# Kernel optimization log

Measured on AMD Instinct MI355X. Metric: run time of the kernel, lower is better.

Reference implementation:

```python
import jax, jax.numpy as jnp
import numpy as np

N = 50000      # nodes
E = 1600000    # edges
F = 128        # num_feature
H = 256        # num_hidden
L = 3          # num_message_passing_steps
EPS = 1e-5     # LayerNorm eps (torch default)


def setup_inputs() -> dict:
    key = jax.random.key(0)
    ks = jax.random.split(key, 8)
    node = jax.random.normal(ks[0], (N, F), dtype=jnp.float32)
    edges = jax.random.randint(ks[1], (2, E), 0, N, dtype=jnp.int64)
    edges_attr = jax.random.uniform(ks[2], (E,), dtype=jnp.float32)
    sF = np.float32(1.0 / np.sqrt(F))
    sH = np.float32(1.0 / np.sqrt(H))
    W1 = jax.random.normal(ks[3], (F, H), dtype=jnp.float32) * sF
    b1 = jnp.zeros((H,), jnp.float32)
    W_convs = jax.random.normal(ks[4], (L, H, H), dtype=jnp.float32) * sH
    b_convs = jnp.zeros((L, H), jnp.float32)
    ln_g = jnp.ones((L, H), jnp.float32)
    ln_b = jnp.zeros((L, H), jnp.float32)
    fc_W = jax.random.normal(ks[5], (H, 2), dtype=jnp.float32) * sH
    fc_b = jnp.zeros((2,), jnp.float32)
    return dict(node=node, edges=edges, edges_attr=edges_attr, W1=W1, b1=b1,
                W_convs=W_convs, b_convs=b_convs, ln_g=ln_g, ln_b=ln_b,
                fc_W=fc_W, fc_b=fc_b)


def gcn_conv(x, src_a, dst_a, w_a, W, b):
    # PyG GCNConv: x' = D^-1/2 (A + I) D^-1/2 (x W) + b, edge weights w.
    # src_a/dst_a/w_a already include self-loops (weight 1).
    n = x.shape[0]
    xw = x @ W                                      # [N, H]
    deg = jax.ops.segment_sum(w_a, dst_a, num_segments=n)
    deg_safe = jnp.where(deg > 0, deg, 1.0)
    dinv = jnp.where(deg > 0, jax.lax.rsqrt(deg_safe), 0.0)
    norm = dinv[src_a] * w_a * dinv[dst_a]          # [E+N]
    msg = xw[src_a] * norm[:, None]                 # gather + scale
    out = jax.ops.segment_sum(msg, dst_a, num_segments=n)  # scatter-add
    return out + b


def layer_norm(x, g, b):
    mu = jnp.mean(x, axis=-1, keepdims=True)
    var = jnp.mean((x - mu) ** 2, axis=-1, keepdims=True)
    return (x - mu) * jax.lax.rsqrt(var + EPS) * g + b


def reference(node, edges, edges_attr, W1, b1, W_convs, b_convs, ln_g, ln_b, fc_W, fc_b):
    n = node.shape[0]
    loop = jnp.arange(n, dtype=edges.dtype)
    src_a = jnp.concatenate([edges[0], loop])
    dst_a = jnp.concatenate([edges[1], loop])
    w_a = jnp.concatenate([edges_attr, jnp.ones((n,), edges_attr.dtype)])

    x = gcn_conv(node, src_a, dst_a, w_a, W1, b1)
    for i in range(L):
        x_res = x
        x = gcn_conv(x, src_a, dst_a, w_a, W_convs[i], b_convs[i])
        x = layer_norm(x, ln_g[i], ln_b[i])
        x = jax.nn.relu(x + x_res)
    x = x @ fc_W + fc_b                              # [N, 2]
    return jnp.mean(x, axis=0, keepdims=True)        # global_mean_pool, batch=None -> [1, 2]
```

## Files before the change

kernel.cpp:

```cpp
#include <hip/hip_runtime.h>

#define EPS 1e-5f
#define FIXSCALE 8388608.0f
#define NBK 64

typedef __attribute__((ext_vector_type(8))) short short8;
typedef __attribute__((ext_vector_type(4))) short short4v;
typedef __attribute__((ext_vector_type(4))) float float4v;
typedef __attribute__((ext_vector_type(2))) float float2v;
typedef __attribute__((ext_vector_type(8))) unsigned short ushort8;
typedef __attribute__((ext_vector_type(4))) unsigned int uint4v;

#if __has_builtin(__builtin_nontemporal_load)
#define NT_LOAD(p) __builtin_nontemporal_load(p)
#else
#define NT_LOAD(p) (*(p))
#endif

__device__ __forceinline__ unsigned short f2b(float f) {
    union { float f; unsigned u; } v; v.f = f;
    unsigned r = v.u + 0x7FFF + ((v.u >> 16) & 1);
    return (unsigned short)(r >> 16);
}
__device__ __forceinline__ float b2f(unsigned short u) {
    union { unsigned u; float f; } v; v.u = ((unsigned)u) << 16;
    return v.f;
}

__device__ __forceinline__ int qbucket(int cnt) {
    int qc = ((cnt + 4) & ~3) >> 2;
    return qc < NBK - 1 ? qc : NBK - 1;
}


__global__ __launch_bounds__(256) void rank_kernel(const int* __restrict__ dst,
                                                   const float* __restrict__ w,
                                                   unsigned long long* __restrict__ combo,
                                                   int* __restrict__ rank, int E) {
    int e = blockIdx.x * 256 + threadIdx.x;
    if (e < E) {
        int d = dst[e];
        unsigned long long pack = (1ULL << 32) | (unsigned long long)(unsigned)(w[e] * FIXSCALE);
        unsigned long long old = atomicAdd(&combo[(size_t)d * 8], pack);
        rank[e] = (int)(old >> 32);
    }
}

__global__ __launch_bounds__(256) void dinv_kernel(const unsigned long long* __restrict__ combo,
                                                   float* __restrict__ dinv, int n) {
    int d = blockIdx.x * 256 + threadIdx.x;
    if (d < n) {
        float degv = (float)(unsigned)(combo[(size_t)d * 8] & 0xffffffffULL) * (1.0f / FIXSCALE);
        dinv[d] = rsqrtf(degv + 1.0f);
    }
}


__global__ __launch_bounds__(256) void bin_hist_kernel(const unsigned long long* __restrict__ combo,
                                                       int* __restrict__ blockhist, int n) {
    __shared__ int lh[NBK];
    int t = threadIdx.x;
    if (t < NBK) lh[t] = 0;
    __syncthreads();
    int d = blockIdx.x * 256 + t;
    if (d < n) {
        int cnt = (int)(combo[(size_t)d * 8] >> 32);
        atomicAdd(&lh[qbucket(cnt)], 1);
    }
    __syncthreads();
    if (t < NBK) blockhist[blockIdx.x * NBK + t] = lh[t];
}

__global__ __launch_bounds__(256) void bin_prescan_kernel(const int* __restrict__ blockhist,
                                                          int* __restrict__ blockpre,
                                                          int* __restrict__ tot, int nblk) {
    int bkt = blockIdx.x;
    int t = threadIdx.x, lane = t & 63, w = t >> 6;
    __shared__ int wsum[4];
    __shared__ int s_carry;
    if (t == 0) s_carry = 0;
    __syncthreads();
    for (int base = 0; base < nblk; base += 256) {
        int i = base + t;
        int v = (i < nblk) ? blockhist[i * NBK + bkt] : 0;
        int x = v;
        for (int off = 1; off < 64; off <<= 1) {
            int u = __shfl_up(x, off);
            if (lane >= off) x += u;
        }
        if (lane == 63) wsum[w] = x;
        __syncthreads();
        if (t == 0) {
            int a = wsum[0];
            wsum[0] = 0;
            for (int k = 1; k < 4; ++k) { int b = wsum[k]; wsum[k] = a; a += b; }
            wsum[0] = 0;
        }
        __syncthreads();
        int carry = s_carry;
        int woff = wsum[w];
        if (i < nblk) blockpre[i * NBK + bkt] = carry + woff + x - v;
        __syncthreads();
        if (t == 255) s_carry = carry + woff + x;
        __syncthreads();
    }
    if (t == 0) tot[bkt] = s_carry;
}

__global__ __launch_bounds__(64) void bin_suffix_kernel(const int* __restrict__ tot,
                                                        int* __restrict__ base) {
    int t = threadIdx.x;
    int v = tot[t];
    int s = v;
    for (int off = 1; off < 64; off <<= 1) {
        int u = __shfl_down(s, off);
        if (t + off < 64) s += u;
    }
    base[t] = s - v;
}

__global__ __launch_bounds__(256) void bin_scatter_kernel(const unsigned long long* __restrict__ combo,
                                                          const int* __restrict__ base,
                                                          const int* __restrict__ blockpre,
                                                          int* __restrict__ perm,
                                                          int* __restrict__ posod,
                                                          int* __restrict__ qlen, int n) {
    __shared__ int lcur[NBK];
    int t = threadIdx.x;
    if (t < NBK) lcur[t] = base[t] + blockpre[blockIdx.x * NBK + t];
    __syncthreads();
    int d = blockIdx.x * 256 + t;
    if (d < n) {
        int cnt = (int)(combo[(size_t)d * 8] >> 32);
        int pos = atomicAdd(&lcur[qbucket(cnt)], 1);
        perm[pos] = d;
        posod[d] = pos;
        qlen[pos] = (cnt + 4) & ~3;
    }
}

__global__ __launch_bounds__(1024) void scan_kernel(const int* __restrict__ qlen,
                                                    int* __restrict__ row_ptr, int n) {
    int tid = threadIdx.x, lane = tid & 63, w = tid >> 6;
    __shared__ int wsum[16];
    __shared__ int s_carry;
    if (tid == 0) s_carry = 0;
    __syncthreads();
    for (int base = 0; base < n; base += 1024) {
        int i = base + tid;
        int v = (i < n) ? qlen[i] : 0;
        int x = v;
        for (int off = 1; off < 64; off <<= 1) {
            int t = __shfl_up(x, off);
            if (lane >= off) x += t;
        }
        if (lane == 63) wsum[w] = x;
        __syncthreads();
        if (w == 0 && lane < 16) {
            int s = wsum[lane];
            for (int off = 1; off < 16; off <<= 1) {
                int t = __shfl_up(s, off, 16);
                if (lane >= off) s += t;
            }
            wsum[lane] = s;
        }
        __syncthreads();
        int carry = s_carry;
        int woff = (w > 0) ? wsum[w - 1] : 0;
        if (i < n) row_ptr[i + 1] = carry + woff + x;
        __syncthreads();
        if (tid == 0) s_carry = carry + wsum[15];
        __syncthreads();
    }
    if (tid == 0) row_ptr[0] = 0;
}

__global__ __launch_bounds__(256) void selfpad_kernel(const unsigned long long* __restrict__ combo,
                                                      const int* __restrict__ row_ptr,
                                                      const int* __restrict__ posod,
                                                      const float* __restrict__ dinv,
                                                      unsigned int* __restrict__ edge, int n) {
    int d = blockIdx.x * 256 + threadIdx.x;
    if (d < n) {
        int cnt = (int)(combo[(size_t)d * 8] >> 32);
        int slot = posod[d];
        int j0 = row_ptr[slot], j1 = row_ptr[slot + 1];
        float di = dinv[d];
        edge[j0] = ((unsigned)f2b(di * di) << 16) | (unsigned)slot;
        for (int j = j0 + 1 + cnt; j < j1; ++j) edge[j] = (unsigned)slot;
    }
}

__global__ __launch_bounds__(256) void scatter2_kernel(
    const int* __restrict__ src, const int* __restrict__ dst,
    const float* __restrict__ w, const int* __restrict__ rank,
    const int* __restrict__ row_ptr, const int* __restrict__ posod,
    const float* __restrict__ dinv, unsigned int* __restrict__ edge, int E) {
    int e = blockIdx.x * 256 + threadIdx.x;
    if (e < E) {
        int d = dst[e], s = src[e];
        float wn = dinv[s] * w[e] * dinv[d];
        edge[row_ptr[posod[d]] + 1 + rank[e]] = ((unsigned)f2b(wn) << 16) | (unsigned)posod[s];
    }
}

__global__ __launch_bounds__(256) void cast_sliced_kernel(const float* __restrict__ in,
                                                          const int* __restrict__ perm,
                                                          unsigned short* __restrict__ out,
                                                          int n, int F) {
    int idx = blockIdx.x * 256 + threadIdx.x;
    if (idx < n * (F / 4)) {
        int f4 = idx * 4;
        int slot = f4 / F, f = f4 - slot * F;
        float4 v = *(const float4*)&in[(size_t)perm[slot] * F + f];
        short4v s = (short4v){(short)f2b(v.x), (short)f2b(v.y), (short)f2b(v.z), (short)f2b(v.w)};
        *(short4v*)&out[((size_t)(f >> 5) * n + slot) * 32 + (f & 31)] = s;
    }
}

__global__ __launch_bounds__(256) void wtrans_kernel(const float* __restrict__ W,
                                                     unsigned short* __restrict__ Wt,
                                                     int K, int Nc) {
    int o = blockIdx.x * 256 + threadIdx.x;
    if (o < K * Nc) {
        int n = o / K, k = o - n * K;
        Wt[o] = f2b(W[(size_t)k * Nc + n]);
    }
}


#define GST 88

template <bool SLICEOUT>
__global__ __launch_bounds__(256) void gemm_n256(const unsigned short* __restrict__ A,
                                                 const unsigned short* __restrict__ Bt,
                                                 unsigned short* __restrict__ Cout,
                                                 const float* __restrict__ bias,
                                                 int M, int K) {
    __shared__ __align__(16) short As[64 * GST];
    __shared__ __align__(16) short Bs[256 * GST];
    int t = threadIdx.x;
    int lane = t & 63, w = t >> 6;
    int quad = lane >> 4, l16 = lane & 15;
    int row0 = blockIdx.x * 64;

    float4v acc[16];
#pragma unroll
    for (int c = 0; c < 16; ++c) acc[c] = (float4v){0.f, 0.f, 0.f, 0.f};

    int arow = t >> 2, ak16 = (t & 3) * 16;
    int bcol0 = t >> 2, bko = (t & 3) * 16;

    for (int k_outer = 0; k_outer < K; k_outer += 64) {
        bool rowok = (row0 + arow) < M;
        const unsigned short* ap = &A[(size_t)(row0 + arow) * K + k_outer + ak16];
        uint4 z = make_uint4(0, 0, 0, 0);
        uint4 u0 = rowok ? *(const uint4*)ap : z;
        uint4 u1 = rowok ? *(const uint4*)(ap + 8) : z;
        *(uint4*)&As[arow * GST + ak16] = u0;
        *(uint4*)&As[arow * GST + ak16 + 8] = u1;
#pragma unroll
        for (int cb = 0; cb < 4; ++cb) {
            int col = bcol0 + 64 * cb;
            const unsigned short* bp = &Bt[(size_t)col * K + k_outer + bko];
#pragma unroll
            for (int u = 0; u < 2; ++u)
                *(uint4*)&Bs[col * GST + bko + u * 8] = *(const uint4*)&bp[u * 8];
        }
        __syncthreads();
#pragma unroll
        for (int k0 = 0; k0 < 64; k0 += 32) {
            short8 a = *(const short8*)&As[(w * 16 + l16) * GST + k0 + quad * 8];
#pragma unroll
            for (int c = 0; c < 16; ++c) {
                short8 b = *(const short8*)&Bs[(c * 16 + l16) * GST + k0 + quad * 8];
                acc[c] = __builtin_amdgcn_mfma_f32_16x16x32_bf16(a, b, acc[c], 0, 0, 0);
            }
        }
        __syncthreads();
    }
#pragma unroll
    for (int c = 0; c < 16; ++c) {
        int col = c * 16 + l16;
        float bcol = (!SLICEOUT) ? bias[col] : 0.0f;
#pragma unroll
        for (int r = 0; r < 4; ++r) {
            int row = row0 + w * 16 + quad * 4 + r;
            if (row < M) {
                if (SLICEOUT)
                    Cout[((size_t)(c >> 1) * M + row) * 32 + ((c & 1) << 4) + l16] = f2b(acc[c][r]);
                else
                    Cout[(size_t)row * 256 + col] = f2b(acc[c][r] + bcol);
            }
        }
    }
}


#define CAPQ 2048

template <int CSH>
__global__ __launch_bounds__(256) void agg_grp(
    const unsigned short* __restrict__ tab0, const int* __restrict__ row_ptr,
    const unsigned int* __restrict__ edge, unsigned short* __restrict__ outb, int n) {
    __shared__ uint4v eq[CAPQ];
    int b = blockIdx.x;
    int s = b & ((1 << CSH) - 1);
    int grp = b >> CSH;
    int t = threadIdx.x;
    int d0 = grp * 64;
    int d = d0 + (t >> 2);

    const uint4v* e4p = (const uint4v*)edge;
    int qbase = row_ptr[d0] >> 2;
    int dmax = d0 + 64 < n ? d0 + 64 : n;
    int qcnt = (row_ptr[dmax] >> 2) - qbase;
    int qstage = qcnt < CAPQ ? qcnt : CAPQ;
    for (int i = t; i < qstage; i += 256) eq[i] = NT_LOAD(&e4p[qbase + i]);
    __syncthreads();

    if (d >= n) return;
    int fo = (t & 3) << 3;
    const unsigned short* tab = tab0 + (size_t)s * n * 32;

    int j = row_ptr[d] >> 2, j1 = row_ptr[d + 1] >> 2;
    int jmid = j1 < qbase + CAPQ ? j1 : qbase + CAPQ;

    float2v a2[4];
#pragma unroll
    for (int k = 0; k < 4; ++k) a2[k] = (float2v){0.f, 0.f};

    auto compq = [&](unsigned e, uint4 r) {
        float wq = __int_as_float((int)(e & 0xffff0000u));
        float2v w2 = {wq, wq};
        float2v f0 = {__uint_as_float(r.x << 16), __uint_as_float(r.x & 0xffff0000u)};
        float2v f1 = {__uint_as_float(r.y << 16), __uint_as_float(r.y & 0xffff0000u)};
        float2v f2 = {__uint_as_float(r.z << 16), __uint_as_float(r.z & 0xffff0000u)};
        float2v f3 = {__uint_as_float(r.w << 16), __uint_as_float(r.w & 0xffff0000u)};
        a2[0] += f0 * w2;
        a2[1] += f1 * w2;
        a2[2] += f2 * w2;
        a2[3] += f3 * w2;
    };
    auto process = [&](uint4v e4) {
#pragma unroll
        for (int u = 0; u < 4; ++u) {
            unsigned e = e4[u];
            unsigned off = ((e & 0xffffu) << 5) + (unsigned)fo;
            uint4 rr = *(const uint4*)(tab + off);
            compq(e, rr);
        }
    };
    auto issue2 = [&](int jj, uint4v& q0, uint4v& q1, uint4* rr) {
        q0 = eq[jj - qbase];
        q1 = eq[jj + 1 - qbase];
#pragma unroll
        for (int u = 0; u < 4; ++u)
            rr[u] = *(const uint4*)(tab + (((q0[u] & 0xffffu) << 5) + (unsigned)fo));
#pragma unroll
        for (int u = 0; u < 4; ++u)
            rr[4 + u] = *(const uint4*)(tab + (((q1[u] & 0xffffu) << 5) + (unsigned)fo));
    };
    auto comp2 = [&](uint4v q0, uint4v q1, const uint4* rr) {
#pragma unroll
        for (int u = 0; u < 4; ++u) compq(q0[u], rr[u]);
#pragma unroll
        for (int u = 0; u < 4; ++u) compq(q1[u], rr[4 + u]);
    };

    uint4v qA0, qA1, qB0, qB1;
    uint4 rrA[8], rrB[8];
    int nq2 = (jmid - j) >> 1;
    if (nq2 > 0) {
        issue2(j, qA0, qA1, rrA);
        int bb = 1;
        for (; bb + 1 < nq2; bb += 2) {
            issue2(j + 2 * bb, qB0, qB1, rrB);
            comp2(qA0, qA1, rrA);
            issue2(j + 2 * bb + 2, qA0, qA1, rrA);
            comp2(qB0, qB1, rrB);
        }
        if (bb < nq2) {
            issue2(j + 2 * bb, qB0, qB1, rrB);
            comp2(qA0, qA1, rrA);
            comp2(qB0, qB1, rrB);
        } else {
            comp2(qA0, qA1, rrA);
        }
        j += 2 * nq2;
    }
    if (j < jmid) { process(eq[j - qbase]); ++j; }
    for (; j < j1; ++j) process(NT_LOAD(&e4p[j]));

    ushort8 o;
#pragma unroll
    for (int k = 0; k < 4; ++k) {
        o[2 * k] = f2b(a2[k].x);
        o[2 * k + 1] = f2b(a2[k].y);
    }
    *(ushort8*)(outb + ((size_t)d << (5 + CSH)) + (s << 5) + fo) = o;
}


__global__ __launch_bounds__(256) void ln_res_relu(
    const unsigned short* __restrict__ preln, const float* __restrict__ bias,
    const float* __restrict__ g, const float* __restrict__ lb,
    const unsigned short* __restrict__ res, unsigned short* __restrict__ out, int n) {
    int wv = __builtin_amdgcn_readfirstlane(threadIdx.x >> 6);
    int d = blockIdx.x * 4 + wv;
    if (d >= n) return;
    int l = threadIdx.x & 63;
    int fo = l * 4;
    ushort4 pv = *(const ushort4*)&preln[(size_t)d * 256 + fo];
    float4 bb = *(const float4*)&bias[fo];
    float v[4] = {b2f(pv.x) + bb.x, b2f(pv.y) + bb.y, b2f(pv.z) + bb.z, b2f(pv.w) + bb.w};
    float s4 = v[0] + v[1] + v[2] + v[3];
#pragma unroll
    for (int off = 1; off < 64; off <<= 1) s4 += __shfl_xor(s4, off);
    float mu = s4 * (1.0f / 256.0f);
    float dv[4];
    float qs = 0.f;
#pragma unroll
    for (int j = 0; j < 4; ++j) { dv[j] = v[j] - mu; qs += dv[j] * dv[j]; }
#pragma unroll
    for (int off = 1; off < 64; off <<= 1) qs += __shfl_xor(qs, off);
    float rs = rsqrtf(qs * (1.0f / 256.0f) + EPS);

    float4 gg = *(const float4*)&g[fo];
    float4 lbv = *(const float4*)&lb[fo];
    ushort4 rr4 = *(const ushort4*)&res[(size_t)d * 256 + fo];
    float ggv[4] = {gg.x, gg.y, gg.z, gg.w};
    float lbvv[4] = {lbv.x, lbv.y, lbv.z, lbv.w};
    float rrv[4] = {b2f(rr4.x), b2f(rr4.y), b2f(rr4.z), b2f(rr4.w)};
    ushort4 o;
    unsigned short* op = (unsigned short*)&o;
#pragma unroll
    for (int j = 0; j < 4; ++j) {
        float x = dv[j] * rs * ggv[j] + lbvv[j] + rrv[j];
        op[j] = f2b(x > 0.f ? x : 0.f);
    }
    *(ushort4*)&out[(size_t)d * 256 + fo] = o;
}


__global__ __launch_bounds__(256) void colsum_kernel(const unsigned short* __restrict__ x,
                                                     float* __restrict__ sums, int n) {
    int h = threadIdx.x;
    float acc = 0.0f;
    for (int r = blockIdx.x; r < n; r += gridDim.x) acc += b2f(x[(size_t)r * 256 + h]);
    atomicAdd(&sums[h], acc);
}

__global__ __launch_bounds__(64) void final_kernel(const float* __restrict__ sums,
                                                   const float* __restrict__ fcW,
                                                   const float* __restrict__ fcb,
                                                   float* __restrict__ out, float invN) {
    int lane = threadIdx.x;
    float p0 = 0.0f, p1 = 0.0f;
    for (int hh = lane; hh < 256; hh += 64) {
        float m = sums[hh];
        p0 += m * fcW[hh * 2 + 0];
        p1 += m * fcW[hh * 2 + 1];
    }
    for (int off = 32; off > 0; off >>= 1) {
        p0 += __shfl_down(p0, off);
        p1 += __shfl_down(p1, off);
    }
    if (lane == 0) {
        out[0] = p0 * invN + fcb[0];
        out[1] = p1 * invN + fcb[1];
    }
}


extern "C" void kernel_launch(void* const* d_in, const int* in_sizes, int n_in,
                              void* d_out, int out_size, void* d_ws, size_t ws_size,
                              hipStream_t stream) {
    const float* node    = (const float*)d_in[0];
    const int*   edges   = (const int*)d_in[1];
    const float* eattr   = (const float*)d_in[2];
    const float* W1      = (const float*)d_in[3];
    const float* b1      = (const float*)d_in[4];
    const float* W_convs = (const float*)d_in[5];
    const float* b_convs = (const float*)d_in[6];
    const float* ln_g    = (const float*)d_in[7];
    const float* ln_b    = (const float*)d_in[8];
    const float* fc_W    = (const float*)d_in[9];
    const float* fc_b    = (const float*)d_in[10];
    float* out = (float*)d_out;

    const int H = in_sizes[4];
    const int F = in_sizes[3] / H;
    const int N = in_sizes[0] / F;
    const int E = in_sizes[2];
    const int L = in_sizes[6] / H;

    const int* src = edges;
    const int* dst = edges + E;

    char* p = (char*)d_ws;
    auto alloc = [&](size_t bytes) {
        char* r = p;
        p += (bytes + 255) & ~(size_t)255;
        return r;
    };
    int nblk = (N + 255) / 256;
    unsigned long long* combo = (unsigned long long*)alloc((size_t)N * 64);
    float* colsums = (float*)alloc((size_t)H * 4);
    size_t zero_bytes = (size_t)((char*)colsums - (char*)combo) + (((size_t)H * 4 + 255) & ~(size_t)255);
    int*   blockhist = (int*)alloc((size_t)nblk * NBK * 4);
    int*   blockpre  = (int*)alloc((size_t)nblk * NBK * 4);
    int*   tot       = (int*)alloc((size_t)NBK * 4);
    int*   bbase     = (int*)alloc((size_t)NBK * 4);
    int*   perm    = (int*)alloc((size_t)N * 4);
    int*   posod   = (int*)alloc((size_t)N * 4);
    int*   qlen    = (int*)alloc((size_t)N * 4);
    float* dinv    = (float*)alloc((size_t)N * 4);
    int*   row_ptr = (int*)alloc((size_t)(N + 1) * 4);
    unsigned int* edge = (unsigned int*)alloc(((size_t)E + 4 * (size_t)N + 64) * 4);
    unsigned short* Wt1 = (unsigned short*)alloc((size_t)H * F * 2);
    unsigned short* Wtc = (unsigned short*)alloc((size_t)L * H * H * 2);
    unsigned short* xw  = (unsigned short*)alloc((size_t)N * H * 2);
    unsigned short* preln = (unsigned short*)alloc((size_t)N * H * 2);
    unsigned short* bufA  = (unsigned short*)alloc((size_t)N * H * 2);
    unsigned short* bufB  = (unsigned short*)alloc((size_t)N * H * 2);
    int*            rank  = (int*)xw;
    unsigned short* nodeb = preln;
    unsigned short* aggn  = preln + (size_t)N * F;

    hipMemsetAsync(combo, 0, zero_bytes, stream);

    int gE = (E + 255) / 256;
    rank_kernel<<<gE, 256, 0, stream>>>(dst, eattr, combo, rank, E);
    dinv_kernel<<<nblk, 256, 0, stream>>>(combo, dinv, N);
    bin_hist_kernel<<<nblk, 256, 0, stream>>>(combo, blockhist, N);
    bin_prescan_kernel<<<NBK, 256, 0, stream>>>(blockhist, blockpre, tot, nblk);
    bin_suffix_kernel<<<1, 64, 0, stream>>>(tot, bbase);
    bin_scatter_kernel<<<nblk, 256, 0, stream>>>(combo, bbase, blockpre, perm, posod, qlen, N);
    scan_kernel<<<1, 1024, 0, stream>>>(qlen, row_ptr, N);
    selfpad_kernel<<<nblk, 256, 0, stream>>>(combo, row_ptr, posod, dinv, edge, N);
    scatter2_kernel<<<gE, 256, 0, stream>>>(src, dst, eattr, rank, row_ptr, posod, dinv, edge, E);

    cast_sliced_kernel<<<(N * (F / 4) + 255) / 256, 256, 0, stream>>>(node, perm, nodeb, N, F);
    wtrans_kernel<<<(F * H + 255) / 256, 256, 0, stream>>>(W1, Wt1, F, H);
    for (int i = 0; i < L; ++i)
        wtrans_kernel<<<(H * H + 255) / 256, 256, 0, stream>>>(
            W_convs + (size_t)i * H * H, Wtc + (size_t)i * H * H, H, H);

    int ngrp64 = (N + 63) / 64;
    int lngrid = (N + 3) / 4;
    int ggrid = (N + 63) / 64;

    agg_grp<2><<<4 * ngrp64, 256, 0, stream>>>(nodeb, row_ptr, edge, aggn, N);
    gemm_n256<false><<<ggrid, 256, 0, stream>>>(aggn, Wt1, bufA, b1, N, F);

    unsigned short* x = bufA;
    unsigned short* other = bufB;
    for (int i = 0; i < L; ++i) {
        gemm_n256<true><<<ggrid, 256, 0, stream>>>(x, Wtc + (size_t)i * H * H, xw, nullptr, N, H);
        agg_grp<3><<<8 * ngrp64, 256, 0, stream>>>(xw, row_ptr, edge, preln, N);
        ln_res_relu<<<lngrid, 256, 0, stream>>>(preln, b_convs + (size_t)i * H,
                                                ln_g + (size_t)i * H, ln_b + (size_t)i * H,
                                                x, other, N);
        unsigned short* t = x; x = other; other = t;
    }

    colsum_kernel<<<256, 256, 0, stream>>>(x, colsums, N);
    final_kernel<<<1, 64, 0, stream>>>(colsums, fc_W, fc_b, out, 1.0f / (float)N);
}
```

Before: 748.2 us.

## Parallelize row-pointer scan across blocks and halve aggregation LDS queue

Replaces the single-block sequential scan over the padded row lengths with a three-phase scan: per-block local scans, a one-wave scan of the block sums, and a parallel add-back pass. This is meant to remove the serialized loop of roughly fifty iterations that ran on one compute unit. It costs two extra kernel launches. Separately, the aggregation kernel's shared-memory edge queue capacity drops from 2048 to 1024 entries, which may raise occupancy but means more groups exceed the staged capacity.

```diff
diff --git a/kernel.cpp b/kernel.cpp
--- a/kernel.cpp
+++ b/kernel.cpp
@@ -139,40 +139,57 @@
     }
 }
 
-__global__ __launch_bounds__(1024) void scan_kernel(const int* __restrict__ qlen,
-                                                    int* __restrict__ row_ptr, int n) {
+
+__global__ __launch_bounds__(1024) void scan_local_kernel(const int* __restrict__ qlen,
+                                                          int* __restrict__ row_ptr,
+                                                          int* __restrict__ bsum, int n) {
     int tid = threadIdx.x, lane = tid & 63, w = tid >> 6;
     __shared__ int wsum[16];
-    __shared__ int s_carry;
-    if (tid == 0) s_carry = 0;
-    __syncthreads();
-    for (int base = 0; base < n; base += 1024) {
-        int i = base + tid;
-        int v = (i < n) ? qlen[i] : 0;
+    int i = blockIdx.x * 1024 + tid;
+    int v = (i < n) ? qlen[i] : 0;
+    int x = v;
+    for (int off = 1; off < 64; off <<= 1) {
+        int t = __shfl_up(x, off);
+        if (lane >= off) x += t;
+    }
+    if (lane == 63) wsum[w] = x;
+    __syncthreads();
+    if (w == 0 && lane < 16) {
+        int s = wsum[lane];
+        for (int off = 1; off < 16; off <<= 1) {
+            int t = __shfl_up(s, off, 16);
+            if (lane >= off) s += t;
+        }
+        wsum[lane] = s;
+    }
+    __syncthreads();
+    int woff = (w > 0) ? wsum[w - 1] : 0;
+    if (i < n) row_ptr[i + 1] = woff + x;
+    if (tid == 0) bsum[blockIdx.x] = wsum[15];
+}
+
+__global__ __launch_bounds__(64) void scan_mid_kernel(int* __restrict__ bsum,
+                                                      int* __restrict__ row_ptr, int nb) {
+    int t = threadIdx.x;
+    int carry = 0;
+    for (int base = 0; base < nb; base += 64) {
+        int idx = base + t;
+        int v = (idx < nb) ? bsum[idx] : 0;
         int x = v;
         for (int off = 1; off < 64; off <<= 1) {
-            int t = __shfl_up(x, off);
-            if (lane >= off) x += t;
-        }
-        if (lane == 63) wsum[w] = x;
-        __syncthreads();
-        if (w == 0 && lane < 16) {
-            int s = wsum[lane];
-            for (int off = 1; off < 16; off <<= 1) {
-                int t = __shfl_up(s, off, 16);
-                if (lane >= off) s += t;
-            }
-            wsum[lane] = s;
-        }
-        __syncthreads();
-        int carry = s_carry;
-        int woff = (w > 0) ? wsum[w - 1] : 0;
-        if (i < n) row_ptr[i + 1] = carry + woff + x;
-        __syncthreads();
-        if (tid == 0) s_carry = carry + wsum[15];
-        __syncthreads();
-    }
-    if (tid == 0) row_ptr[0] = 0;
+            int u = __shfl_up(x, off);
+            if (t >= off) x += u;
+        }
+        if (idx < nb) bsum[idx] = carry + x - v;
+        carry += __shfl(x, 63);
+    }
+    if (t == 0) row_ptr[0] = 0;
+}
+
+__global__ __launch_bounds__(1024) void scan_add_kernel(const int* __restrict__ bsum,
+                                                        int* __restrict__ row_ptr, int n) {
+    int i = blockIdx.x * 1024 + threadIdx.x;
+    if (i < n) row_ptr[i + 1] += bsum[blockIdx.x];
 }
 
 __global__ __launch_bounds__(256) void selfpad_kernel(const unsigned long long* __restrict__ combo,
@@ -297,7 +314,7 @@
 }
 
 
-#define CAPQ 2048
+#define CAPQ 1024
 
 template <int CSH>
 __global__ __launch_bounds__(256) void agg_grp(
@@ -505,6 +522,7 @@
         return r;
     };
     int nblk = (N + 255) / 256;
+    int nb1024 = (N + 1023) / 1024;
     unsigned long long* combo = (unsigned long long*)alloc((size_t)N * 64);
     float* colsums = (float*)alloc((size_t)H * 4);
     size_t zero_bytes = (size_t)((char*)colsums - (char*)combo) + (((size_t)H * 4 + 255) & ~(size_t)255);
@@ -517,6 +535,7 @@
     int*   qlen    = (int*)alloc((size_t)N * 4);
     float* dinv    = (float*)alloc((size_t)N * 4);
     int*   row_ptr = (int*)alloc((size_t)(N + 1) * 4);
+    int*   bsum    = (int*)alloc((size_t)nb1024 * 4);
     unsigned int* edge = (unsigned int*)alloc(((size_t)E + 4 * (size_t)N + 64) * 4);
     unsigned short* Wt1 = (unsigned short*)alloc((size_t)H * F * 2);
     unsigned short* Wtc = (unsigned short*)alloc((size_t)L * H * H * 2);
@@ -537,7 +556,9 @@
     bin_prescan_kernel<<<NBK, 256, 0, stream>>>(blockhist, blockpre, tot, nblk);
     bin_suffix_kernel<<<1, 64, 0, stream>>>(tot, bbase);
     bin_scatter_kernel<<<nblk, 256, 0, stream>>>(combo, bbase, blockpre, perm, posod, qlen, N);
-    scan_kernel<<<1, 1024, 0, stream>>>(qlen, row_ptr, N);
+    scan_local_kernel<<<nb1024, 1024, 0, stream>>>(qlen, row_ptr, bsum, N);
+    scan_mid_kernel<<<1, 64, 0, stream>>>(bsum, row_ptr, nb1024);
+    scan_add_kernel<<<nb1024, 1024, 0, stream>>>(bsum, row_ptr, N);
     selfpad_kernel<<<nblk, 256, 0, stream>>>(combo, row_ptr, posod, dinv, edge, N);
     scatter2_kernel<<<gE, 256, 0, stream>>>(src, dst, eattr, rank, row_ptr, posod, dinv, edge, E);
 
```

Measured after the change: 712.8 us. 4.7% less time.
